# Kernel tuning notes

Measured on AMD Instinct MI355X. Metric: run time of the kernel, lower is better.

## Reference

```python
import jax, jax.numpy as jnp
import numpy as np

_EPS = 1e-4  # pytorch3d se3_exp_map clamps the SQUARED rotation angle at this eps


def _hat(w):
    # w: [..., 3] -> skew-symmetric [..., 3, 3]
    wx, wy, wz = w[..., 0], w[..., 1], w[..., 2]
    z = jnp.zeros_like(wx)
    return jnp.stack([
        jnp.stack([z, -wz, wy], axis=-1),
        jnp.stack([wz, z, -wx], axis=-1),
        jnp.stack([-wy, wx, z], axis=-1),
    ], axis=-2)


def _se3_exp(dofs):
    # dofs: [..., 6] = (log_translation, log_rotation), pytorch3d convention.
    # Returns R [..., 3, 3] and t [..., 3] such that p' = R @ p + t,
    # matching pytorch3d's row-convention matrix M ([:3,:3]=R^T, [3,:3]=t)
    # applied as p' = p @ M[:3,:3] + M[3,:3].
    t_log = dofs[..., :3]
    w = dofs[..., 3:]
    nrms = jnp.sum(w * w, axis=-1)
    theta = jnp.sqrt(jnp.clip(nrms, _EPS))  # [...]
    H = _hat(w)
    H2 = H @ H
    st, ct = jnp.sin(theta), jnp.cos(theta)
    f1 = (st / theta)[..., None, None]
    f2 = ((1.0 - ct) / (theta * theta))[..., None, None]
    f3 = ((theta - st) / (theta * theta * theta))[..., None, None]
    I = jnp.eye(3, dtype=dofs.dtype)
    R = I + f1 * H + f2 * H2            # Rodrigues
    V = I + f2 * H + f3 * H2            # left-Jacobian of SO(3)
    t = jnp.einsum('...ij,...j->...i', V, t_log)
    return R, t


def setup_inputs() -> dict:
    key = jax.random.key(0)
    k1, k2 = jax.random.split(key)
    B, T, N = 64, 28, 4096
    X_v = jax.random.normal(k1, (B, T, N, 3), dtype=jnp.float32)
    dofs = jax.random.normal(k2, (B, T, 6), dtype=jnp.float32)
    return {"X_v": X_v, "dofs": dofs}


def reference(X_v, dofs):
    # Fused, fully-batched version of the per-tooth python loop:
    # one SE3 exp over all (B,T) transforms + one batched point transform.
    R, t = _se3_exp(dofs)                                  # [B,T,3,3], [B,T,3]
    out = jnp.einsum('btij,btnj->btni', R, X_v) + t[:, :, None, :]
    return out
```

## Files before the change

### kernel.cpp

```cpp
#include <hip/hip_runtime.h>


__device__ __forceinline__ float rfl(float x) {
    return __uint_as_float(__builtin_amdgcn_readfirstlane(__float_as_uint(x)));
}

__global__ __launch_bounds__(256) void se3_apply_kernel(
    const float* __restrict__ X,
    const float* __restrict__ dofs,
    float* __restrict__ out,
    int n3,
    int tilesPerBT)
{
    const int bt   = blockIdx.x / tilesPerBT;
    const int tile = blockIdx.x - bt * tilesPerBT;
    const int t    = threadIdx.x;

    const int fInBT = tile * 3072 + t * 12;
    const long long baseF = (long long)bt * (long long)n3 + (long long)fInBT;
    const float4* __restrict__ Xp = (const float4*)(X + baseF);
    float4* __restrict__ Op       = (float4*)(out + baseF);

    const bool full = (fInBT + 12) <= n3;
    float4 v0, v1, v2;
    if (full) { v0 = Xp[0]; v1 = Xp[1]; v2 = Xp[2]; }

    const float* d = dofs + bt * 6;
    const float tx = d[0], ty = d[1], tz = d[2];
    const float wx = d[3], wy = d[4], wz = d[5];

    const float nrm2  = wx * wx + wy * wy + wz * wz;
    const float th2   = fmaxf(nrm2, 1e-4f);
    const float theta = sqrtf(th2);
    const float st = sinf(theta);
    const float ct = cosf(theta);
    const float f1 = st / theta;
    const float f2 = (1.0f - ct) / th2;
    const float f3 = (theta - st) / (th2 * theta);

    const float xx = wx * wx, yy = wy * wy, zz = wz * wz;
    const float xy = wx * wy, xz = wx * wz, yz = wy * wz;

    const float R00 = rfl(1.0f - f2 * (yy + zz));
    const float R01 = rfl(f2 * xy - f1 * wz);
    const float R02 = rfl(f2 * xz + f1 * wy);
    const float R10 = rfl(f2 * xy + f1 * wz);
    const float R11 = rfl(1.0f - f2 * (xx + zz));
    const float R12 = rfl(f2 * yz - f1 * wx);
    const float R20 = rfl(f2 * xz - f1 * wy);
    const float R21 = rfl(f2 * yz + f1 * wx);
    const float R22 = rfl(1.0f - f2 * (xx + yy));

    const float V00 = 1.0f - f3 * (yy + zz);
    const float V01 = f3 * xy - f2 * wz;
    const float V02 = f3 * xz + f2 * wy;
    const float V10 = f3 * xy + f2 * wz;
    const float V11 = 1.0f - f3 * (xx + zz);
    const float V12 = f3 * yz - f2 * wx;
    const float V20 = f3 * xz - f2 * wy;
    const float V21 = f3 * yz + f2 * wx;
    const float V22 = 1.0f - f3 * (xx + yy);

    const float Tx = rfl(V00 * tx + V01 * ty + V02 * tz);
    const float Ty = rfl(V10 * tx + V11 * ty + V12 * tz);
    const float Tz = rfl(V20 * tx + V21 * ty + V22 * tz);

    if (full) {
        const float x0 = v0.x, y0 = v0.y, z0 = v0.z;
        const float x1 = v0.w, y1 = v1.x, z1 = v1.y;
        const float x2 = v1.z, y2 = v1.w, z2 = v2.x;
        const float x3 = v2.y, y3 = v2.z, z3 = v2.w;

        float4 o0, o1, o2;
        o0.x = fmaf(R00, x0, fmaf(R01, y0, fmaf(R02, z0, Tx)));
        o0.y = fmaf(R10, x0, fmaf(R11, y0, fmaf(R12, z0, Ty)));
        o0.z = fmaf(R20, x0, fmaf(R21, y0, fmaf(R22, z0, Tz)));
        o0.w = fmaf(R00, x1, fmaf(R01, y1, fmaf(R02, z1, Tx)));
        o1.x = fmaf(R10, x1, fmaf(R11, y1, fmaf(R12, z1, Ty)));
        o1.y = fmaf(R20, x1, fmaf(R21, y1, fmaf(R22, z1, Tz)));
        o1.z = fmaf(R00, x2, fmaf(R01, y2, fmaf(R02, z2, Tx)));
        o1.w = fmaf(R10, x2, fmaf(R11, y2, fmaf(R12, z2, Ty)));
        o2.x = fmaf(R20, x2, fmaf(R21, y2, fmaf(R22, z2, Tz)));
        o2.y = fmaf(R00, x3, fmaf(R01, y3, fmaf(R02, z3, Tx)));
        o2.z = fmaf(R10, x3, fmaf(R11, y3, fmaf(R12, z3, Ty)));
        o2.w = fmaf(R20, x3, fmaf(R21, y3, fmaf(R22, z3, Tz)));

        Op[0] = o0; Op[1] = o1; Op[2] = o2;
    } else {
        for (int f = fInBT; f + 3 <= n3; f += 3) {
            const long long g = (long long)bt * (long long)n3 + f;
            const float px = X[g + 0], py = X[g + 1], pz = X[g + 2];
            out[g + 0] = fmaf(R00, px, fmaf(R01, py, fmaf(R02, pz, Tx)));
            out[g + 1] = fmaf(R10, px, fmaf(R11, py, fmaf(R12, pz, Ty)));
            out[g + 2] = fmaf(R20, px, fmaf(R21, py, fmaf(R22, pz, Tz)));
        }
    }
}

extern "C" void kernel_launch(void* const* d_in, const int* in_sizes, int n_in,
                              void* d_out, int out_size, void* d_ws, size_t ws_size,
                              hipStream_t stream) {
    const float* X    = (const float*)d_in[0];
    const float* dofs = (const float*)d_in[1];
    float* out        = (float*)d_out;

    const int BT = in_sizes[1] / 6;
    const int n3 = in_sizes[0] / BT;

    const int tilesPerBT = (n3 + 3071) / 3072;

    dim3 grid((unsigned)(BT * tilesPerBT));
    se3_apply_kernel<<<grid, 256, 0, stream>>>(X, dofs, out, n3, tilesPerBT);
}
```

Before: 158.5 us.

## Use one block per transform with double-buffered register prefetch over tiles

The launch now uses one block per (B,T) transform instead of one block per 3072-float tile. Each block computes the SE3 exponential once and loops over its tiles. Inputs for the next tiles are prefetched into two alternating register sets, so loads overlap with the FMAs and stores. This removes the repeated per-tile recomputation of R and t. In exchange the grid has fewer, longer-running blocks, which may reduce memory-level parallelism and latency hiding for this bandwidth-bound copy-like kernel.

```diff
diff --git a/kernel.cpp b/kernel.cpp
--- a/kernel.cpp
+++ b/kernel.cpp
@@ -9,21 +9,25 @@
     const float* __restrict__ X,
     const float* __restrict__ dofs,
     float* __restrict__ out,
-    int n3,
-    int tilesPerBT)
+    int n3)
 {
-    const int bt   = blockIdx.x / tilesPerBT;
-    const int tile = blockIdx.x - bt * tilesPerBT;
-    const int t    = threadIdx.x;
+    const int bt = blockIdx.x;
+    const int t  = threadIdx.x;
+    const long long base = (long long)bt * (long long)n3;
+    const int nIter = (n3 + 3071) / 3072;
+    const int f4    = t * 3;
+    const int slotF = t * 12;
 
-    const int fInBT = tile * 3072 + t * 12;
-    const long long baseF = (long long)bt * (long long)n3 + (long long)fInBT;
-    const float4* __restrict__ Xp = (const float4*)(X + baseF);
-    float4* __restrict__ Op       = (float4*)(out + baseF);
+    const float4* __restrict__ Xp = (const float4*)(X + base);
+    float4*       __restrict__ Op = (float4*)(out + base);
 
-    const bool full = (fInBT + 12) <= n3;
-    float4 v0, v1, v2;
-    if (full) { v0 = Xp[0]; v1 = Xp[1]; v2 = Xp[2]; }
+    float4 a0, a1, a2, b0, b1, b2;
+    if ((slotF + 12) <= n3) {
+        a0 = Xp[f4]; a1 = Xp[f4 + 1]; a2 = Xp[f4 + 2];
+    }
+    if (nIter > 1 && (3072 + slotF + 12) <= n3) {
+        b0 = Xp[768 + f4]; b1 = Xp[768 + f4 + 1]; b2 = Xp[768 + f4 + 2];
+    }
 
     const float* d = dofs + bt * 6;
     const float tx = d[0], ty = d[1], tz = d[2];
@@ -65,7 +69,7 @@
     const float Ty = rfl(V10 * tx + V11 * ty + V12 * tz);
     const float Tz = rfl(V20 * tx + V21 * ty + V22 * tz);
 
-    if (full) {
+    auto xform = [&](const float4& v0, const float4& v1, const float4& v2, int of) {
         const float x0 = v0.x, y0 = v0.y, z0 = v0.z;
         const float x1 = v0.w, y1 = v1.x, z1 = v1.y;
         const float x2 = v1.z, y2 = v1.w, z2 = v2.x;
@@ -85,14 +89,33 @@
         o2.z = fmaf(R10, x3, fmaf(R11, y3, fmaf(R12, z3, Ty)));
         o2.w = fmaf(R20, x3, fmaf(R21, y3, fmaf(R22, z3, Tz)));
 
-        Op[0] = o0; Op[1] = o1; Op[2] = o2;
-    } else {
-        for (int f = fInBT; f + 3 <= n3; f += 3) {
-            const long long g = (long long)bt * (long long)n3 + f;
-            const float px = X[g + 0], py = X[g + 1], pz = X[g + 2];
-            out[g + 0] = fmaf(R00, px, fmaf(R01, py, fmaf(R02, pz, Tx)));
-            out[g + 1] = fmaf(R10, px, fmaf(R11, py, fmaf(R12, pz, Ty)));
-            out[g + 2] = fmaf(R20, px, fmaf(R21, py, fmaf(R22, pz, Tz)));
+        Op[of] = o0; Op[of + 1] = o1; Op[of + 2] = o2;
+    };
+
+    for (int k = 0; k < nIter; k += 2) {
+        if ((k * 3072 + slotF + 12) <= n3)
+            xform(a0, a1, a2, k * 768 + f4);
+        if ((k + 2) < nIter && ((k + 2) * 3072 + slotF + 12) <= n3) {
+            const int p = (k + 2) * 768 + f4;
+            a0 = Xp[p]; a1 = Xp[p + 1]; a2 = Xp[p + 2];
+        }
+        if ((k + 1) < nIter) {
+            if (((k + 1) * 3072 + slotF + 12) <= n3)
+                xform(b0, b1, b2, (k + 1) * 768 + f4);
+            if ((k + 3) < nIter && ((k + 3) * 3072 + slotF + 12) <= n3) {
+                const int p = (k + 3) * 768 + f4;
+                b0 = Xp[p]; b1 = Xp[p + 1]; b2 = Xp[p + 2];
+            }
+        }
+    }
+
+    const int myLast = (nIter - 1) * 3072 + slotF;
+    if (myLast < n3 && (myLast + 12) > n3) {
+        for (int f = myLast; f + 3 <= n3; f += 3) {
+            const float px = X[base + f], py = X[base + f + 1], pz = X[base + f + 2];
+            out[base + f + 0] = fmaf(R00, px, fmaf(R01, py, fmaf(R02, pz, Tx)));
+            out[base + f + 1] = fmaf(R10, px, fmaf(R11, py, fmaf(R12, pz, Ty)));
+            out[base + f + 2] = fmaf(R20, px, fmaf(R21, py, fmaf(R22, pz, Tz)));
         }
     }
 }
@@ -107,8 +130,6 @@
     const int BT = in_sizes[1] / 6;
     const int n3 = in_sizes[0] / BT;
 
-    const int tilesPerBT = (n3 + 3071) / 3072;
-
-    dim3 grid((unsigned)(BT * tilesPerBT));
-    se3_apply_kernel<<<grid, 256, 0, stream>>>(X, dofs, out, n3, tilesPerBT);
+    dim3 grid((unsigned)BT);
+    se3_apply_kernel<<<grid, 256, 0, stream>>>(X, dofs, out, n3);
 }
```

After: 161.4 us. Within noise of the previous version (+1.9%).
